# Performance work log

Hardware: AMD Instinct MI355X
Metric: run time of the kernel (lower is better)

## Reference

```python
import jax, jax.numpy as jnp
import numpy as np


def setup_inputs() -> dict:
    key = jax.random.key(0)
    ks = jax.random.split(key, 10)
    T, B, L, E, D, V = 4, 64, 32, 1024, 256, 32000
    sentences = jax.random.randint(ks[0], (T, B, L), 0, V)
    lengths = jax.random.randint(ks[1], (T, B), 4, L + 1)
    embed = jax.random.normal(ks[2], (V, D), dtype=jnp.float32) * 0.1
    pos_w = jax.random.uniform(ks[3], (L, D), dtype=jnp.float32)
    keys = jax.random.normal(ks[4], (B, E, D), dtype=jnp.float32) * 0.1
    entities = jax.random.normal(ks[5], (B, E, D), dtype=jnp.float32) * 0.1
    Wk = jax.random.normal(ks[6], (D, D), dtype=jnp.float32) * 0.05
    Wv = jax.random.normal(ks[7], (D, D), dtype=jnp.float32) * 0.05
    Wc = jax.random.normal(ks[8], (D, D), dtype=jnp.float32) * 0.05
    prelu_w = jnp.ones((D,), dtype=jnp.float32)  # PReLU weight init to 1 per source
    return {"embed": embed, "pos_w": pos_w, "keys": keys, "entities": entities,
            "Wk": Wk, "Wv": Wv, "Wc": Wc, "prelu_w": prelu_w,
            "sentences": sentences, "lengths": lengths}


def reference(embed, pos_w, keys, entities, Wk, Wv, Wc, prelu_w, sentences, lengths):
    # keys are detached in EntNet when opt.lk is True
    keys = jax.lax.stop_gradient(keys)
    T, B, L = sentences.shape
    pos = jnp.arange(L)

    def prelu(x):
        return jnp.where(x >= 0, x, prelu_w * x)

    def step(ents, inp):
        sent, lens = inp  # [B,L], [B]
        # SentenceEncoder: positional-mask weighted bag of words
        w = embed[sent]  # [B,L,D]
        mask = (pos[None, :] < lens[:, None]).astype(w.dtype)[:, :, None]
        h = jnp.sum(w * pos_w[None] * mask, axis=1)  # [B,D]
        # EntitySelector (DoubleAttention, sigmoid): gate on both entities and keys
        scores = jnp.einsum('bd,bed->be', h, ents) + jnp.einsum('bd,bed->be', h, keys)
        dist = jax.nn.sigmoid(scores)[:, :, None]  # [B,E,1] broadcast of n_dist
        # EntityUpdater components
        ok = jnp.einsum('bed,df->bef', keys, Wk)
        oe = jnp.einsum('bed,df->bef', ents, Wv)
        oc = (h @ Wc)[:, None, :]  # [B,1,D] broadcast over entities
        pre = ok + oe + oc
        # afunc without 'n', act != 'I': gated PReLU update
        new = dist * prelu(pre) + (1.0 - dist) * ents
        # L2 renormalization per entity vector
        new = new / jnp.linalg.norm(new, axis=2, keepdims=True)
        joint = jnp.sum(dist * new, axis=1)  # [B,D]
        return new, joint

    ents, joints = jax.lax.scan(step, entities, (sentences, lengths))
    return ents, joints[-1]
```

## Files before the change

### kernel.cpp

```cpp
#include <hip/hip_runtime.h>
#include <cmath>

constexpr int T = 4, B = 64, L = 32, E = 1024, D = 256;
constexpr int MT = 32;
constexpr int NBLK = E / MT;

typedef __attribute__((ext_vector_type(8))) short short8;
typedef __attribute__((ext_vector_type(4))) float f32x4;
typedef __attribute__((ext_vector_type(4))) unsigned short u16x4;

static __device__ __forceinline__ unsigned short f2bf(float x) {
  unsigned int u = __builtin_bit_cast(unsigned int, x);
  unsigned int r = u + 0x7fffu + ((u >> 16) & 1u);
  return (unsigned short)(r >> 16);
}
static __device__ __forceinline__ float bf2f(unsigned short s) {
  unsigned int u = ((unsigned int)s) << 16;
  return __builtin_bit_cast(float, u);
}

__global__ void k_h(const float* __restrict__ embed, const float* __restrict__ pos_w,
                    const int* __restrict__ sentences, const int* __restrict__ lengths,
                    float* __restrict__ h) {
  int tb = blockIdx.x;
  int d  = threadIdx.x;
  const int* sent = sentences + tb * L;
  int len = lengths[tb];
  float acc = 0.f;
  for (int l = 0; l < len; ++l) {
    int tok = sent[l];
    acc += embed[(size_t)tok * D + d] * pos_w[l * D + d];
  }
  h[(size_t)tb * D + d] = acc;
}

__global__ void k_oc(const float* __restrict__ h, const float* __restrict__ Wc,
                     float* __restrict__ oc) {
  int tb = blockIdx.x;
  int f  = threadIdx.x;
  __shared__ float hs[D];
  hs[f] = h[(size_t)tb * D + f];
  __syncthreads();
  float acc = 0.f;
  for (int d0 = 0; d0 < D; d0 += 4) {
    float4 hv = *(const float4*)&hs[d0];
    acc += hv.x * Wc[(d0 + 0) * D + f] + hv.y * Wc[(d0 + 1) * D + f]
         + hv.z * Wc[(d0 + 2) * D + f] + hv.w * Wc[(d0 + 3) * D + f];
  }
  oc[(size_t)tb * D + f] = acc;
}

__global__ void k_wt(const float* __restrict__ Wv, const float* __restrict__ Wk,
                     unsigned short* __restrict__ Wvfrag,
                     unsigned short* __restrict__ Wkfrag) {
  int n = blockIdx.x, k = threadIdx.x;
  int idx = (((n >> 4) * 8 + (k >> 5)) * 64 + ((k >> 3) & 3) * 16 + (n & 15)) * 8 + (k & 7);
  Wvfrag[idx] = f2bf(Wv[(size_t)k * D + n]);
  Wkfrag[idx] = f2bf(Wk[(size_t)k * D + n]);
}

__global__ __launch_bounds__(256, 3) void k_scan(
    const float* __restrict__ entities,
    const float* __restrict__ keys,
    const unsigned short* __restrict__ Wvfrag,
    const unsigned short* __restrict__ Wkfrag,
    const float* __restrict__ h,
    const float* __restrict__ oc,
    const float* __restrict__ prelu_w,
    float* __restrict__ out_ents,
    float* __restrict__ joint) {
  int b = blockIdx.y, e0 = blockIdx.x * MT;
  int tid = threadIdx.x;
  int lane = tid & 63, w = tid >> 6;
  int col16 = lane & 15, kg = lane >> 4;
  const int aswz = (col16 & 7) << 3;

  __shared__ unsigned short es[MT * D];
  __shared__ unsigned short oks[MT * D];
  __shared__ float hs4[T][D];
  __shared__ float ocs4[T][D];
  __shared__ float pws[D];
  __shared__ float ksc_s[T][MT];
  __shared__ float dist_s[MT];
  __shared__ float red0[4][MT], red1[4][MT];
  __shared__ float inv_s[MT];

#pragma unroll
  for (int t = 0; t < T; ++t) {
    hs4[t][tid]  = h[((size_t)t * B + b) * D + tid];
    ocs4[t][tid] = oc[((size_t)t * B + b) * D + tid];
  }
  pws[tid] = prelu_w[tid];
  __syncthreads();

  {
    int r = tid >> 3, c0 = (tid & 7) * 32;
    const float4* src = (const float4*)(keys + ((size_t)b * E + e0 + r) * D + c0);
    float p[T] = {0.f, 0.f, 0.f, 0.f};
#pragma unroll
    for (int ch = 0; ch < 4; ++ch) {
      float4 v0 = src[ch * 2], v1 = src[ch * 2 + 1];
      int c = c0 + ch * 8;
#pragma unroll
      for (int t = 0; t < T; ++t) {
        p[t] += v0.x * hs4[t][c]     + v0.y * hs4[t][c + 1]
              + v0.z * hs4[t][c + 2] + v0.w * hs4[t][c + 3]
              + v1.x * hs4[t][c + 4] + v1.y * hs4[t][c + 5]
              + v1.z * hs4[t][c + 6] + v1.w * hs4[t][c + 7];
      }
      unsigned short u[8];
      u[0] = f2bf(v0.x); u[1] = f2bf(v0.y); u[2] = f2bf(v0.z); u[3] = f2bf(v0.w);
      u[4] = f2bf(v1.x); u[5] = f2bf(v1.y); u[6] = f2bf(v1.z); u[7] = f2bf(v1.w);
      int idx = (r * D + c) ^ ((r & 7) << 3);
      *(short8*)&es[idx] = *(const short8*)&u[0];
    }
#pragma unroll
    for (int t = 0; t < T; ++t) {
      p[t] += __shfl_xor(p[t], 1);
      p[t] += __shfl_xor(p[t], 2);
      p[t] += __shfl_xor(p[t], 4);
    }
    if ((tid & 7) == 0) {
#pragma unroll
      for (int t = 0; t < T; ++t) ksc_s[t][r] = p[t];
    }
  }
  __syncthreads();

  {
    f32x4 acc[2][4];
#pragma unroll
    for (int rt = 0; rt < 2; ++rt)
#pragma unroll
      for (int ct = 0; ct < 4; ++ct) acc[rt][ct] = (f32x4)(0.f);
#pragma unroll 2
    for (int kb = 0; kb < 8; ++kb) {
      int k0 = kb * 32 + kg * 8;
      short8 a[2];
#pragma unroll
      for (int rt = 0; rt < 2; ++rt)
        a[rt] = *(const short8*)&es[((rt * 16 + col16) * D + k0) ^ aswz];
      short8 bv[4];
#pragma unroll
      for (int ct = 0; ct < 4; ++ct)
        bv[ct] = *(const short8*)&Wkfrag[(size_t)(((w * 4 + ct) * 8 + kb) * 64 + lane) * 8];
#pragma unroll
      for (int rt = 0; rt < 2; ++rt)
#pragma unroll
        for (int ct = 0; ct < 4; ++ct)
          acc[rt][ct] = __builtin_amdgcn_mfma_f32_16x16x32_bf16(a[rt], bv[ct], acc[rt][ct], 0, 0, 0);
    }
#pragma unroll
    for (int rt = 0; rt < 2; ++rt)
#pragma unroll
      for (int ct = 0; ct < 4; ++ct) {
        u16x4 o;
#pragma unroll
        for (int r = 0; r < 4; ++r) o[r] = f2bf(acc[rt][ct][r]);
        *(u16x4*)&oks[(((w * 2 + rt) * 4 + ct) * 64 + lane) * 4] = o;
      }
  }
  __syncthreads();

  {
    int r = tid >> 3, c0 = (tid & 7) * 32;
    const float4* src = (const float4*)(entities + ((size_t)b * E + e0 + r) * D + c0);
    float p = 0.f;
#pragma unroll
    for (int ch = 0; ch < 4; ++ch) {
      float4 v0 = src[ch * 2], v1 = src[ch * 2 + 1];
      int c = c0 + ch * 8;
      p += v0.x * hs4[0][c]     + v0.y * hs4[0][c + 1]
         + v0.z * hs4[0][c + 2] + v0.w * hs4[0][c + 3]
         + v1.x * hs4[0][c + 4] + v1.y * hs4[0][c + 5]
         + v1.z * hs4[0][c + 6] + v1.w * hs4[0][c + 7];
      unsigned short u[8];
      u[0] = f2bf(v0.x); u[1] = f2bf(v0.y); u[2] = f2bf(v0.z); u[3] = f2bf(v0.w);
      u[4] = f2bf(v1.x); u[5] = f2bf(v1.y); u[6] = f2bf(v1.z); u[7] = f2bf(v1.w);
      int idx = (r * D + c) ^ ((r & 7) << 3);
      *(short8*)&es[idx] = *(const short8*)&u[0];
    }
    p += __shfl_xor(p, 1);
    p += __shfl_xor(p, 2);
    p += __shfl_xor(p, 4);
    if ((tid & 7) == 0)
      dist_s[r] = 1.f / (1.f + expf(-(p + ksc_s[0][r])));
  }
  __syncthreads();

  size_t obase = ((size_t)b * E + e0) * D;
#pragma unroll
  for (int t = 0; t < T; ++t) {
    f32x4 acc[2][4];
#pragma unroll
    for (int rt = 0; rt < 2; ++rt)
#pragma unroll
      for (int ct = 0; ct < 4; ++ct) acc[rt][ct] = (f32x4)(0.f);
#pragma unroll 2
    for (int kb = 0; kb < 8; ++kb) {
      int k0 = kb * 32 + kg * 8;
      short8 a[2];
#pragma unroll
      for (int rt = 0; rt < 2; ++rt)
        a[rt] = *(const short8*)&es[((rt * 16 + col16) * D + k0) ^ aswz];
      short8 bv[4];
#pragma unroll
      for (int ct = 0; ct < 4; ++ct)
        bv[ct] = *(const short8*)&Wvfrag[(size_t)(((w * 4 + ct) * 8 + kb) * 64 + lane) * 8];
#pragma unroll
      for (int rt = 0; rt < 2; ++rt)
#pragma unroll
        for (int ct = 0; ct < 4; ++ct)
          acc[rt][ct] = __builtin_amdgcn_mfma_f32_16x16x32_bf16(a[rt], bv[ct], acc[rt][ct], 0, 0, 0);
    }

#pragma unroll
    for (int rt = 0; rt < 2; ++rt)
#pragma unroll
      for (int ct = 0; ct < 4; ++ct) {
        int n = w * 64 + ct * 16 + col16;
        float ocv = ocs4[t][n], pwv = pws[n];
        u16x4 ok4 = *(const u16x4*)&oks[(((w * 2 + rt) * 4 + ct) * 64 + lane) * 4];
#pragma unroll
        for (int r = 0; r < 4; ++r) {
          int m = rt * 16 + kg * 4 + r;
          float pre = acc[rt][ct][r] + ocv + bf2f(ok4[r]);
          float pr = pre >= 0.f ? pre : pwv * pre;
          float de = dist_s[m];
          float ev = bf2f(es[(m * D + n) ^ ((m & 7) << 3)]);
          acc[rt][ct][r] = de * pr + (1.f - de) * ev;
        }
      }

#pragma unroll
    for (int rt = 0; rt < 2; ++rt)
#pragma unroll
      for (int r = 0; r < 4; ++r) {
        float s = acc[rt][0][r] * acc[rt][0][r] + acc[rt][1][r] * acc[rt][1][r]
                + acc[rt][2][r] * acc[rt][2][r] + acc[rt][3][r] * acc[rt][3][r];
        float dn = 0.f;
        if (t < 3) {
#pragma unroll
          for (int ct = 0; ct < 4; ++ct) {
            int n = w * 64 + ct * 16 + col16;
            dn += acc[rt][ct][r] * hs4[t + 1 < T ? t + 1 : 0][n];
          }
        }
        s += __shfl_xor(s, 1); s += __shfl_xor(s, 2);
        s += __shfl_xor(s, 4); s += __shfl_xor(s, 8);
        if (t < 3) {
          dn += __shfl_xor(dn, 1); dn += __shfl_xor(dn, 2);
          dn += __shfl_xor(dn, 4); dn += __shfl_xor(dn, 8);
        }
        if (col16 == 0) {
          int m = rt * 16 + kg * 4 + r;
          red0[w][m] = s;
          red1[w][m] = dn;
        }
      }
    __syncthreads();
    if (tid < MT) {
      float ss = red0[0][tid] + red0[1][tid] + red0[2][tid] + red0[3][tid];
      float iv = rsqrtf(ss);
      inv_s[tid] = iv;
      if (t < 3) {
        float dd = red1[0][tid] + red1[1][tid] + red1[2][tid] + red1[3][tid];
        dist_s[tid] = 1.f / (1.f + expf(-(iv * dd + ksc_s[t + 1 < T ? t + 1 : 0][tid])));
      }
    }
    __syncthreads();

    if (t < 3) {
#pragma unroll
      for (int rt = 0; rt < 2; ++rt)
#pragma unroll
        for (int ct = 0; ct < 4; ++ct) {
          int n = w * 64 + ct * 16 + col16;
#pragma unroll
          for (int r = 0; r < 4; ++r) {
            int m = rt * 16 + kg * 4 + r;
            es[(m * D + n) ^ ((m & 7) << 3)] = f2bf(acc[rt][ct][r] * inv_s[m]);
          }
        }
    } else {
      float jacc[4] = {0.f, 0.f, 0.f, 0.f};
#pragma unroll
      for (int rt = 0; rt < 2; ++rt)
#pragma unroll
        for (int ct = 0; ct < 4; ++ct) {
          int n = w * 64 + ct * 16 + col16;
#pragma unroll
          for (int r = 0; r < 4; ++r) {
            int m = rt * 16 + kg * 4 + r;
            float val = acc[rt][ct][r] * inv_s[m];
            out_ents[obase + (size_t)m * D + n] = val;
            jacc[ct] += dist_s[m] * val;
          }
        }
#pragma unroll
      for (int ct = 0; ct < 4; ++ct) {
        float s = jacc[ct];
        s += __shfl_xor(s, 16);
        s += __shfl_xor(s, 32);
        if (kg == 0) atomicAdd(&joint[(size_t)b * D + w * 64 + ct * 16 + col16], s);
      }
    }
    __syncthreads();
  }
}

extern "C" void kernel_launch(void* const* d_in, const int* in_sizes, int n_in,
                              void* d_out, int out_size, void* d_ws, size_t ws_size,
                              hipStream_t stream) {
  const float* embed    = (const float*)d_in[0];
  const float* pos_w    = (const float*)d_in[1];
  const float* keys     = (const float*)d_in[2];
  const float* entities = (const float*)d_in[3];
  const float* Wk       = (const float*)d_in[4];
  const float* Wv       = (const float*)d_in[5];
  const float* Wc       = (const float*)d_in[6];
  const float* prelu_w  = (const float*)d_in[7];
  const int* sentences  = (const int*)d_in[8];
  const int* lengths    = (const int*)d_in[9];

  float* out_ents  = (float*)d_out;
  float* out_joint = out_ents + (size_t)B * E * D;

  float* h  = (float*)d_ws;
  float* oc = h + (size_t)T * B * D;
  unsigned short* Wvfrag = (unsigned short*)(oc + (size_t)T * B * D);
  unsigned short* Wkfrag = Wvfrag + (size_t)D * D;

  hipMemsetAsync(out_joint, 0, (size_t)B * D * sizeof(float), stream);

  k_h<<<T * B, D, 0, stream>>>(embed, pos_w, sentences, lengths, h);
  k_oc<<<T * B, D, 0, stream>>>(h, Wc, oc);
  k_wt<<<D, D, 0, stream>>>(Wv, Wk, Wvfrag, Wkfrag);

  dim3 grid(NBLK, B);
  k_scan<<<grid, 256, 0, stream>>>(entities, keys, Wvfrag, Wkfrag,
                                   h, oc, prelu_w, out_ents, out_joint);

  (void)in_sizes; (void)n_in; (void)out_size; (void)ws_size;
}
```

Before: 140.5 us.

## Compute attention scores via extra MFMA column instead of scalar dot products

The h·keys and h·entities score dot products move from scalar FMAs over fp32 shared h into an extra MFMA per row tile, with h stored as bf16 in the B operand (four timesteps in four columns). The next-step dist is now computed after each step's MFMA from the bf16 entity tile, rather than from the fp32 unnormalized update plus a separate reduction. h and oc are kept in shared memory as bf16, which shrinks LDS use and may raise occupancy. This adds one MFMA per row tile per k-block and an extra barrier per step, and it lowers the precision of the scores to bf16.

```diff
diff --git a/kernel.cpp b/kernel.cpp
--- a/kernel.cpp
+++ b/kernel.cpp
@@ -77,18 +77,18 @@
 
   __shared__ unsigned short es[MT * D];
   __shared__ unsigned short oks[MT * D];
-  __shared__ float hs4[T][D];
-  __shared__ float ocs4[T][D];
+  __shared__ unsigned short hbf[T * D];
+  __shared__ unsigned short ocb[T * D];
   __shared__ float pws[D];
   __shared__ float ksc_s[T][MT];
   __shared__ float dist_s[MT];
-  __shared__ float red0[4][MT], red1[4][MT];
+  __shared__ float red0[4][MT];
   __shared__ float inv_s[MT];
 
 #pragma unroll
   for (int t = 0; t < T; ++t) {
-    hs4[t][tid]  = h[((size_t)t * B + b) * D + tid];
-    ocs4[t][tid] = oc[((size_t)t * B + b) * D + tid];
+    hbf[t * D + tid] = f2bf(h[((size_t)t * B + b) * D + tid]);
+    ocb[t * D + tid] = f2bf(oc[((size_t)t * B + b) * D + tid]);
   }
   pws[tid] = prelu_w[tid];
   __syncthreads();
@@ -96,43 +96,26 @@
   {
     int r = tid >> 3, c0 = (tid & 7) * 32;
     const float4* src = (const float4*)(keys + ((size_t)b * E + e0 + r) * D + c0);
-    float p[T] = {0.f, 0.f, 0.f, 0.f};
 #pragma unroll
     for (int ch = 0; ch < 4; ++ch) {
       float4 v0 = src[ch * 2], v1 = src[ch * 2 + 1];
-      int c = c0 + ch * 8;
-#pragma unroll
-      for (int t = 0; t < T; ++t) {
-        p[t] += v0.x * hs4[t][c]     + v0.y * hs4[t][c + 1]
-              + v0.z * hs4[t][c + 2] + v0.w * hs4[t][c + 3]
-              + v1.x * hs4[t][c + 4] + v1.y * hs4[t][c + 5]
-              + v1.z * hs4[t][c + 6] + v1.w * hs4[t][c + 7];
-      }
       unsigned short u[8];
       u[0] = f2bf(v0.x); u[1] = f2bf(v0.y); u[2] = f2bf(v0.z); u[3] = f2bf(v0.w);
       u[4] = f2bf(v1.x); u[5] = f2bf(v1.y); u[6] = f2bf(v1.z); u[7] = f2bf(v1.w);
-      int idx = (r * D + c) ^ ((r & 7) << 3);
+      int idx = (r * D + c0 + ch * 8) ^ ((r & 7) << 3);
       *(short8*)&es[idx] = *(const short8*)&u[0];
     }
-#pragma unroll
-    for (int t = 0; t < T; ++t) {
-      p[t] += __shfl_xor(p[t], 1);
-      p[t] += __shfl_xor(p[t], 2);
-      p[t] += __shfl_xor(p[t], 4);
-    }
-    if ((tid & 7) == 0) {
-#pragma unroll
-      for (int t = 0; t < T; ++t) ksc_s[t][r] = p[t];
-    }
   }
   __syncthreads();
 
   {
-    f32x4 acc[2][4];
-#pragma unroll
-    for (int rt = 0; rt < 2; ++rt)
+    f32x4 acc[2][4], hacc[2];
+#pragma unroll
+    for (int rt = 0; rt < 2; ++rt) {
+      hacc[rt] = (f32x4)(0.f);
 #pragma unroll
       for (int ct = 0; ct < 4; ++ct) acc[rt][ct] = (f32x4)(0.f);
+    }
 #pragma unroll 2
     for (int kb = 0; kb < 8; ++kb) {
       int k0 = kb * 32 + kg * 8;
@@ -140,62 +123,64 @@
 #pragma unroll
       for (int rt = 0; rt < 2; ++rt)
         a[rt] = *(const short8*)&es[((rt * 16 + col16) * D + k0) ^ aswz];
+      short8 hv = (short8)(0);
+      if (col16 < 4) hv = *(const short8*)&hbf[col16 * D + k0];
       short8 bv[4];
 #pragma unroll
       for (int ct = 0; ct < 4; ++ct)
         bv[ct] = *(const short8*)&Wkfrag[(size_t)(((w * 4 + ct) * 8 + kb) * 64 + lane) * 8];
 #pragma unroll
-      for (int rt = 0; rt < 2; ++rt)
+      for (int rt = 0; rt < 2; ++rt) {
 #pragma unroll
         for (int ct = 0; ct < 4; ++ct)
           acc[rt][ct] = __builtin_amdgcn_mfma_f32_16x16x32_bf16(a[rt], bv[ct], acc[rt][ct], 0, 0, 0);
+        hacc[rt] = __builtin_amdgcn_mfma_f32_16x16x32_bf16(a[rt], hv, hacc[rt], 0, 0, 0);
+      }
     }
 #pragma unroll
     for (int rt = 0; rt < 2; ++rt)
 #pragma unroll
       for (int ct = 0; ct < 4; ++ct) {
-        u16x4 o;
-#pragma unroll
-        for (int r = 0; r < 4; ++r) o[r] = f2bf(acc[rt][ct][r]);
+        unsigned short o0 = f2bf(acc[rt][ct][0]), o1 = f2bf(acc[rt][ct][1]);
+        unsigned short o2 = f2bf(acc[rt][ct][2]), o3 = f2bf(acc[rt][ct][3]);
+        u16x4 o = { o0, o1, o2, o3 };
         *(u16x4*)&oks[(((w * 2 + rt) * 4 + ct) * 64 + lane) * 4] = o;
       }
+    if (w == 0 && col16 < 4) {
+#pragma unroll
+      for (int rt = 0; rt < 2; ++rt)
+#pragma unroll
+        for (int r = 0; r < 4; ++r)
+          ksc_s[col16][rt * 16 + kg * 4 + r] = hacc[rt][r];
+    }
   }
   __syncthreads();
 
   {
     int r = tid >> 3, c0 = (tid & 7) * 32;
     const float4* src = (const float4*)(entities + ((size_t)b * E + e0 + r) * D + c0);
-    float p = 0.f;
 #pragma unroll
     for (int ch = 0; ch < 4; ++ch) {
       float4 v0 = src[ch * 2], v1 = src[ch * 2 + 1];
-      int c = c0 + ch * 8;
-      p += v0.x * hs4[0][c]     + v0.y * hs4[0][c + 1]
-         + v0.z * hs4[0][c + 2] + v0.w * hs4[0][c + 3]
-         + v1.x * hs4[0][c + 4] + v1.y * hs4[0][c + 5]
-         + v1.z * hs4[0][c + 6] + v1.w * hs4[0][c + 7];
       unsigned short u[8];
       u[0] = f2bf(v0.x); u[1] = f2bf(v0.y); u[2] = f2bf(v0.z); u[3] = f2bf(v0.w);
       u[4] = f2bf(v1.x); u[5] = f2bf(v1.y); u[6] = f2bf(v1.z); u[7] = f2bf(v1.w);
-      int idx = (r * D + c) ^ ((r & 7) << 3);
+      int idx = (r * D + c0 + ch * 8) ^ ((r & 7) << 3);
       *(short8*)&es[idx] = *(const short8*)&u[0];
     }
-    p += __shfl_xor(p, 1);
-    p += __shfl_xor(p, 2);
-    p += __shfl_xor(p, 4);
-    if ((tid & 7) == 0)
-      dist_s[r] = 1.f / (1.f + expf(-(p + ksc_s[0][r])));
   }
   __syncthreads();
 
   size_t obase = ((size_t)b * E + e0) * D;
 #pragma unroll
   for (int t = 0; t < T; ++t) {
-    f32x4 acc[2][4];
-#pragma unroll
-    for (int rt = 0; rt < 2; ++rt)
+    f32x4 acc[2][4], hacc[2];
+#pragma unroll
+    for (int rt = 0; rt < 2; ++rt) {
+      hacc[rt] = (f32x4)(0.f);
 #pragma unroll
       for (int ct = 0; ct < 4; ++ct) acc[rt][ct] = (f32x4)(0.f);
+    }
 #pragma unroll 2
     for (int kb = 0; kb < 8; ++kb) {
       int k0 = kb * 32 + kg * 8;
@@ -203,23 +188,38 @@
 #pragma unroll
       for (int rt = 0; rt < 2; ++rt)
         a[rt] = *(const short8*)&es[((rt * 16 + col16) * D + k0) ^ aswz];
+      short8 hv = (short8)(0);
+      if (col16 < 4) hv = *(const short8*)&hbf[col16 * D + k0];
       short8 bv[4];
 #pragma unroll
       for (int ct = 0; ct < 4; ++ct)
         bv[ct] = *(const short8*)&Wvfrag[(size_t)(((w * 4 + ct) * 8 + kb) * 64 + lane) * 8];
 #pragma unroll
-      for (int rt = 0; rt < 2; ++rt)
+      for (int rt = 0; rt < 2; ++rt) {
 #pragma unroll
         for (int ct = 0; ct < 4; ++ct)
           acc[rt][ct] = __builtin_amdgcn_mfma_f32_16x16x32_bf16(a[rt], bv[ct], acc[rt][ct], 0, 0, 0);
-    }
+        hacc[rt] = __builtin_amdgcn_mfma_f32_16x16x32_bf16(a[rt], hv, hacc[rt], 0, 0, 0);
+      }
+    }
+
+    if (w == 0 && col16 == t) {
+#pragma unroll
+      for (int rt = 0; rt < 2; ++rt)
+#pragma unroll
+        for (int r = 0; r < 4; ++r) {
+          int m = rt * 16 + kg * 4 + r;
+          dist_s[m] = 1.f / (1.f + expf(-(hacc[rt][r] + ksc_s[t][m])));
+        }
+    }
+    __syncthreads();
 
 #pragma unroll
     for (int rt = 0; rt < 2; ++rt)
 #pragma unroll
       for (int ct = 0; ct < 4; ++ct) {
         int n = w * 64 + ct * 16 + col16;
-        float ocv = ocs4[t][n], pwv = pws[n];
+        float ocv = bf2f(ocb[t * D + n]), pwv = pws[n];
         u16x4 ok4 = *(const u16x4*)&oks[(((w * 2 + rt) * 4 + ct) * 64 + lane) * 4];
 #pragma unroll
         for (int r = 0; r < 4; ++r) {
@@ -238,36 +238,13 @@
       for (int r = 0; r < 4; ++r) {
         float s = acc[rt][0][r] * acc[rt][0][r] + acc[rt][1][r] * acc[rt][1][r]
                 + acc[rt][2][r] * acc[rt][2][r] + acc[rt][3][r] * acc[rt][3][r];
-        float dn = 0.f;
-        if (t < 3) {
-#pragma unroll
-          for (int ct = 0; ct < 4; ++ct) {
-            int n = w * 64 + ct * 16 + col16;
-            dn += acc[rt][ct][r] * hs4[t + 1 < T ? t + 1 : 0][n];
-          }
-        }
         s += __shfl_xor(s, 1); s += __shfl_xor(s, 2);
         s += __shfl_xor(s, 4); s += __shfl_xor(s, 8);
-        if (t < 3) {
-          dn += __shfl_xor(dn, 1); dn += __shfl_xor(dn, 2);
-          dn += __shfl_xor(dn, 4); dn += __shfl_xor(dn, 8);
-        }
-        if (col16 == 0) {
-          int m = rt * 16 + kg * 4 + r;
-          red0[w][m] = s;
-          red1[w][m] = dn;
-        }
+        if (col16 == 0) red0[w][rt * 16 + kg * 4 + r] = s;
       }
     __syncthreads();
-    if (tid < MT) {
-      float ss = red0[0][tid] + red0[1][tid] + red0[2][tid] + red0[3][tid];
-      float iv = rsqrtf(ss);
-      inv_s[tid] = iv;
-      if (t < 3) {
-        float dd = red1[0][tid] + red1[1][tid] + red1[2][tid] + red1[3][tid];
-        dist_s[tid] = 1.f / (1.f + expf(-(iv * dd + ksc_s[t + 1 < T ? t + 1 : 0][tid])));
-      }
-    }
+    if (tid < MT)
+      inv_s[tid] = rsqrtf(red0[0][tid] + red0[1][tid] + red0[2][tid] + red0[3][tid]);
     __syncthreads();
 
     if (t < 3) {
@@ -282,6 +259,7 @@
             es[(m * D + n) ^ ((m & 7) << 3)] = f2bf(acc[rt][ct][r] * inv_s[m]);
           }
         }
+      __syncthreads();
     } else {
       float jacc[4] = {0.f, 0.f, 0.f, 0.f};
 #pragma unroll
@@ -305,7 +283,6 @@
         if (kg == 0) atomicAdd(&joint[(size_t)b * D + w * 64 + ct * 16 + col16], s);
       }
     }
-    __syncthreads();
   }
 }
 
@@ -331,7 +308,7 @@
   unsigned short* Wvfrag = (unsigned short*)(oc + (size_t)T * B * D);
   unsigned short* Wkfrag = Wvfrag + (size_t)D * D;
 
-  hipMemsetAsync(out_joint, 0, (size_t)B * D * sizeof(float), stream);
+  (void)hipMemsetAsync(out_joint, 0, (size_t)B * D * sizeof(float), stream);
 
   k_h<<<T * B, D, 0, stream>>>(embed, pos_w, sentences, lengths, h);
   k_oc<<<T * B, D, 0, stream>>>(h, Wc, oc);
```

New measurement: 152.6 us. +8.6%, slower.

## Use 512-thread blocks in scan kernel and keep key projection in registers

Applied to the files above, without the earlier changes.

Doubles the scan kernel's block to 8 waves, so each wave covers 32 output columns instead of 64 and the row-loading phases use 16 threads per row. The bf16 keys·Wk result now stays in registers instead of a shared-memory buffer, which cuts shared memory per block and removes an LDS round trip. The aim is more waves in flight per CU to hide memory and MFMA latency. In exchange, the cross-wave reductions have twice as many partials, the B-fragment loads are spread over more waves, and the trailing barrier of each step is restructured.

```diff
diff --git a/kernel.cpp b/kernel.cpp
--- a/kernel.cpp
+++ b/kernel.cpp
@@ -59,7 +59,7 @@
   Wkfrag[idx] = f2bf(Wk[(size_t)k * D + n]);
 }
 
-__global__ __launch_bounds__(256, 3) void k_scan(
+__global__ __launch_bounds__(512) void k_scan(
     const float* __restrict__ entities,
     const float* __restrict__ keys,
     const unsigned short* __restrict__ Wvfrag,
@@ -76,29 +76,33 @@
   const int aswz = (col16 & 7) << 3;
 
   __shared__ unsigned short es[MT * D];
-  __shared__ unsigned short oks[MT * D];
   __shared__ float hs4[T][D];
   __shared__ float ocs4[T][D];
   __shared__ float pws[D];
   __shared__ float ksc_s[T][MT];
   __shared__ float dist_s[MT];
-  __shared__ float red0[4][MT], red1[4][MT];
+  __shared__ float red0[8][MT], red1[8][MT];
   __shared__ float inv_s[MT];
 
-#pragma unroll
-  for (int t = 0; t < T; ++t) {
-    hs4[t][tid]  = h[((size_t)t * B + b) * D + tid];
-    ocs4[t][tid] = oc[((size_t)t * B + b) * D + tid];
-  }
-  pws[tid] = prelu_w[tid];
-  __syncthreads();
-
   {
-    int r = tid >> 3, c0 = (tid & 7) * 32;
+    int c = tid & 255;
+    if (tid < 256) {
+#pragma unroll
+      for (int t = 0; t < T; ++t) hs4[t][c] = h[((size_t)t * B + b) * D + c];
+      pws[c] = prelu_w[c];
+    } else {
+#pragma unroll
+      for (int t = 0; t < T; ++t) ocs4[t][c] = oc[((size_t)t * B + b) * D + c];
+    }
+  }
+  __syncthreads();
+
+  {
+    int r = tid >> 4, c0 = (tid & 15) * 16;
     const float4* src = (const float4*)(keys + ((size_t)b * E + e0 + r) * D + c0);
     float p[T] = {0.f, 0.f, 0.f, 0.f};
 #pragma unroll
-    for (int ch = 0; ch < 4; ++ch) {
+    for (int ch = 0; ch < 2; ++ch) {
       float4 v0 = src[ch * 2], v1 = src[ch * 2 + 1];
       int c = c0 + ch * 8;
 #pragma unroll
@@ -119,20 +123,22 @@
       p[t] += __shfl_xor(p[t], 1);
       p[t] += __shfl_xor(p[t], 2);
       p[t] += __shfl_xor(p[t], 4);
-    }
-    if ((tid & 7) == 0) {
+      p[t] += __shfl_xor(p[t], 8);
+    }
+    if ((tid & 15) == 0) {
 #pragma unroll
       for (int t = 0; t < T; ++t) ksc_s[t][r] = p[t];
     }
   }
   __syncthreads();
 
+  u16x4 okc[2][2];
   {
-    f32x4 acc[2][4];
-#pragma unroll
-    for (int rt = 0; rt < 2; ++rt)
-#pragma unroll
-      for (int ct = 0; ct < 4; ++ct) acc[rt][ct] = (f32x4)(0.f);
+    f32x4 acc[2][2];
+#pragma unroll
+    for (int rt = 0; rt < 2; ++rt)
+#pragma unroll
+      for (int ct = 0; ct < 2; ++ct) acc[rt][ct] = (f32x4)(0.f);
 #pragma unroll 2
     for (int kb = 0; kb < 8; ++kb) {
       int k0 = kb * 32 + kg * 8;
@@ -140,34 +146,33 @@
 #pragma unroll
       for (int rt = 0; rt < 2; ++rt)
         a[rt] = *(const short8*)&es[((rt * 16 + col16) * D + k0) ^ aswz];
-      short8 bv[4];
-#pragma unroll
-      for (int ct = 0; ct < 4; ++ct)
-        bv[ct] = *(const short8*)&Wkfrag[(size_t)(((w * 4 + ct) * 8 + kb) * 64 + lane) * 8];
-#pragma unroll
-      for (int rt = 0; rt < 2; ++rt)
-#pragma unroll
-        for (int ct = 0; ct < 4; ++ct)
+      short8 bv[2];
+#pragma unroll
+      for (int ct = 0; ct < 2; ++ct)
+        bv[ct] = *(const short8*)&Wkfrag[(size_t)(((w * 2 + ct) * 8 + kb) * 64 + lane) * 8];
+#pragma unroll
+      for (int rt = 0; rt < 2; ++rt)
+#pragma unroll
+        for (int ct = 0; ct < 2; ++ct)
           acc[rt][ct] = __builtin_amdgcn_mfma_f32_16x16x32_bf16(a[rt], bv[ct], acc[rt][ct], 0, 0, 0);
     }
 #pragma unroll
     for (int rt = 0; rt < 2; ++rt)
 #pragma unroll
-      for (int ct = 0; ct < 4; ++ct) {
-        u16x4 o;
-#pragma unroll
-        for (int r = 0; r < 4; ++r) o[r] = f2bf(acc[rt][ct][r]);
-        *(u16x4*)&oks[(((w * 2 + rt) * 4 + ct) * 64 + lane) * 4] = o;
+      for (int ct = 0; ct < 2; ++ct) {
+        u16x4 o = { f2bf(acc[rt][ct][0]), f2bf(acc[rt][ct][1]),
+                    f2bf(acc[rt][ct][2]), f2bf(acc[rt][ct][3]) };
+        okc[rt][ct] = o;
       }
   }
   __syncthreads();
 
   {
-    int r = tid >> 3, c0 = (tid & 7) * 32;
+    int r = tid >> 4, c0 = (tid & 15) * 16;
     const float4* src = (const float4*)(entities + ((size_t)b * E + e0 + r) * D + c0);
     float p = 0.f;
 #pragma unroll
-    for (int ch = 0; ch < 4; ++ch) {
+    for (int ch = 0; ch < 2; ++ch) {
       float4 v0 = src[ch * 2], v1 = src[ch * 2 + 1];
       int c = c0 + ch * 8;
       p += v0.x * hs4[0][c]     + v0.y * hs4[0][c + 1]
@@ -183,7 +188,8 @@
     p += __shfl_xor(p, 1);
     p += __shfl_xor(p, 2);
     p += __shfl_xor(p, 4);
-    if ((tid & 7) == 0)
+    p += __shfl_xor(p, 8);
+    if ((tid & 15) == 0)
       dist_s[r] = 1.f / (1.f + expf(-(p + ksc_s[0][r])));
   }
   __syncthreads();
@@ -191,11 +197,11 @@
   size_t obase = ((size_t)b * E + e0) * D;
 #pragma unroll
   for (int t = 0; t < T; ++t) {
-    f32x4 acc[2][4];
-#pragma unroll
-    for (int rt = 0; rt < 2; ++rt)
-#pragma unroll
-      for (int ct = 0; ct < 4; ++ct) acc[rt][ct] = (f32x4)(0.f);
+    f32x4 acc[2][2];
+#pragma unroll
+    for (int rt = 0; rt < 2; ++rt)
+#pragma unroll
+      for (int ct = 0; ct < 2; ++ct) acc[rt][ct] = (f32x4)(0.f);
 #pragma unroll 2
     for (int kb = 0; kb < 8; ++kb) {
       int k0 = kb * 32 + kg * 8;
@@ -203,24 +209,24 @@
 #pragma unroll
       for (int rt = 0; rt < 2; ++rt)
         a[rt] = *(const short8*)&es[((rt * 16 + col16) * D + k0) ^ aswz];
-      short8 bv[4];
-#pragma unroll
-      for (int ct = 0; ct < 4; ++ct)
-        bv[ct] = *(const short8*)&Wvfrag[(size_t)(((w * 4 + ct) * 8 + kb) * 64 + lane) * 8];
-#pragma unroll
-      for (int rt = 0; rt < 2; ++rt)
-#pragma unroll
-        for (int ct = 0; ct < 4; ++ct)
+      short8 bv[2];
+#pragma unroll
+      for (int ct = 0; ct < 2; ++ct)
+        bv[ct] = *(const short8*)&Wvfrag[(size_t)(((w * 2 + ct) * 8 + kb) * 64 + lane) * 8];
+#pragma unroll
+      for (int rt = 0; rt < 2; ++rt)
+#pragma unroll
+        for (int ct = 0; ct < 2; ++ct)
           acc[rt][ct] = __builtin_amdgcn_mfma_f32_16x16x32_bf16(a[rt], bv[ct], acc[rt][ct], 0, 0, 0);
     }
 
 #pragma unroll
     for (int rt = 0; rt < 2; ++rt)
 #pragma unroll
-      for (int ct = 0; ct < 4; ++ct) {
-        int n = w * 64 + ct * 16 + col16;
+      for (int ct = 0; ct < 2; ++ct) {
+        int n = w * 32 + ct * 16 + col16;
         float ocv = ocs4[t][n], pwv = pws[n];
-        u16x4 ok4 = *(const u16x4*)&oks[(((w * 2 + rt) * 4 + ct) * 64 + lane) * 4];
+        u16x4 ok4 = okc[rt][ct];
 #pragma unroll
         for (int r = 0; r < 4; ++r) {
           int m = rt * 16 + kg * 4 + r;
@@ -236,13 +242,12 @@
     for (int rt = 0; rt < 2; ++rt)
 #pragma unroll
       for (int r = 0; r < 4; ++r) {
-        float s = acc[rt][0][r] * acc[rt][0][r] + acc[rt][1][r] * acc[rt][1][r]
-                + acc[rt][2][r] * acc[rt][2][r] + acc[rt][3][r] * acc[rt][3][r];
+        float s = acc[rt][0][r] * acc[rt][0][r] + acc[rt][1][r] * acc[rt][1][r];
         float dn = 0.f;
         if (t < 3) {
 #pragma unroll
-          for (int ct = 0; ct < 4; ++ct) {
-            int n = w * 64 + ct * 16 + col16;
+          for (int ct = 0; ct < 2; ++ct) {
+            int n = w * 32 + ct * 16 + col16;
             dn += acc[rt][ct][r] * hs4[t + 1 < T ? t + 1 : 0][n];
           }
         }
@@ -260,13 +265,13 @@
       }
     __syncthreads();
     if (tid < MT) {
-      float ss = red0[0][tid] + red0[1][tid] + red0[2][tid] + red0[3][tid];
+      float ss = 0.f, dd = 0.f;
+#pragma unroll
+      for (int ww = 0; ww < 8; ++ww) { ss += red0[ww][tid]; dd += red1[ww][tid]; }
       float iv = rsqrtf(ss);
       inv_s[tid] = iv;
-      if (t < 3) {
-        float dd = red1[0][tid] + red1[1][tid] + red1[2][tid] + red1[3][tid];
+      if (t < 3)
         dist_s[tid] = 1.f / (1.f + expf(-(iv * dd + ksc_s[t + 1 < T ? t + 1 : 0][tid])));
-      }
     }
     __syncthreads();
 
@@ -274,21 +279,22 @@
 #pragma unroll
       for (int rt = 0; rt < 2; ++rt)
 #pragma unroll
-        for (int ct = 0; ct < 4; ++ct) {
-          int n = w * 64 + ct * 16 + col16;
+        for (int ct = 0; ct < 2; ++ct) {
+          int n = w * 32 + ct * 16 + col16;
 #pragma unroll
           for (int r = 0; r < 4; ++r) {
             int m = rt * 16 + kg * 4 + r;
             es[(m * D + n) ^ ((m & 7) << 3)] = f2bf(acc[rt][ct][r] * inv_s[m]);
           }
         }
+      __syncthreads();
     } else {
-      float jacc[4] = {0.f, 0.f, 0.f, 0.f};
-#pragma unroll
-      for (int rt = 0; rt < 2; ++rt)
-#pragma unroll
-        for (int ct = 0; ct < 4; ++ct) {
-          int n = w * 64 + ct * 16 + col16;
+      float jacc[2] = {0.f, 0.f};
+#pragma unroll
+      for (int rt = 0; rt < 2; ++rt)
+#pragma unroll
+        for (int ct = 0; ct < 2; ++ct) {
+          int n = w * 32 + ct * 16 + col16;
 #pragma unroll
           for (int r = 0; r < 4; ++r) {
             int m = rt * 16 + kg * 4 + r;
@@ -298,14 +304,13 @@
           }
         }
 #pragma unroll
-      for (int ct = 0; ct < 4; ++ct) {
+      for (int ct = 0; ct < 2; ++ct) {
         float s = jacc[ct];
         s += __shfl_xor(s, 16);
         s += __shfl_xor(s, 32);
-        if (kg == 0) atomicAdd(&joint[(size_t)b * D + w * 64 + ct * 16 + col16], s);
-      }
-    }
-    __syncthreads();
+        if (kg == 0) atomicAdd(&joint[(size_t)b * D + w * 32 + ct * 16 + col16], s);
+      }
+    }
   }
 }
 
@@ -331,14 +336,14 @@
   unsigned short* Wvfrag = (unsigned short*)(oc + (size_t)T * B * D);
   unsigned short* Wkfrag = Wvfrag + (size_t)D * D;
 
-  hipMemsetAsync(out_joint, 0, (size_t)B * D * sizeof(float), stream);
+  (void)hipMemsetAsync(out_joint, 0, (size_t)B * D * sizeof(float), stream);
 
   k_h<<<T * B, D, 0, stream>>>(embed, pos_w, sentences, lengths, h);
   k_oc<<<T * B, D, 0, stream>>>(h, Wc, oc);
   k_wt<<<D, D, 0, stream>>>(Wv, Wk, Wvfrag, Wkfrag);
 
   dim3 grid(NBLK, B);
-  k_scan<<<grid, 256, 0, stream>>>(entities, keys, Wvfrag, Wkfrag,
+  k_scan<<<grid, 512, 0, stream>>>(entities, keys, Wvfrag, Wkfrag,
                                    h, oc, prelu_w, out_ents, out_joint);
 
   (void)in_sizes; (void)n_in; (void)out_size; (void)ws_size;
```

New measurement: 149.7 us. 1.07x slower.
